# Performance work log

Hardware: AMD Instinct MI355X
Metric: run time of the kernel (lower is better)

## Reference

```python
import jax, jax.numpy as jnp
import numpy as np

EPS = 1e-7  # keras backend epsilon used inside compute_ciou
MAX_MATCHES = 10
ALPHA = 0.5
BETA = 6.0
EPSILON = 1e-9


def compute_ciou(b1, b2):
    # b1, b2: broadcastable (..., 4) boxes in xyxy format
    x_min1, y_min1, x_max1, y_max1 = (b1[..., 0], b1[..., 1], b1[..., 2], b1[..., 3])
    x_min2, y_min2, x_max2, y_max2 = (b2[..., 0], b2[..., 1], b2[..., 2], b2[..., 3])
    w1 = x_max1 - x_min1
    h1 = y_max1 - y_min1 + EPS
    w2 = x_max2 - x_min2
    h2 = y_max2 - y_min2 + EPS
    inter = (jnp.maximum(jnp.minimum(x_max1, x_max2) - jnp.maximum(x_min1, x_min2), 0.0)
             * jnp.maximum(jnp.minimum(y_max1, y_max2) - jnp.maximum(y_min1, y_min2), 0.0))
    union = w1 * h1 + w2 * h2 - inter + EPS
    iou = inter / union
    cw = jnp.maximum(x_max1, x_max2) - jnp.minimum(x_min1, x_min2)
    ch = jnp.maximum(y_max1, y_max2) - jnp.minimum(y_min1, y_min2)
    c2 = cw * cw + ch * ch + EPS
    rho2 = ((x_min2 + x_max2 - x_min1 - x_max1) ** 2
            + (y_min2 + y_max2 - y_min1 - y_max1) ** 2) / 4.0
    v = (4.0 / (np.pi ** 2)) * (jnp.arctan(w2 / h2) - jnp.arctan(w1 / h1)) ** 2
    alpha = v / (v - iou + (1.0 + EPS))
    return iou - (rho2 / c2 + v * alpha)


def setup_inputs() -> dict:
    key = jax.random.key(0)
    B, A, C, G = 32, 8400, 80, 100
    ks = jax.random.split(key, 5)
    # Class scores in (0,1), as after sigmoid head (power(., 0.5) needs >=0).
    scores = jax.nn.sigmoid(jax.random.normal(ks[0], (B, A, C), jnp.float32))
    anchors = jax.random.uniform(ks[1], (A, 2), jnp.float32, 0.0, 640.0)

    def rand_boxes(k, shape):
        k1, k2 = jax.random.split(k)
        xy1 = jax.random.uniform(k1, shape + (2,), jnp.float32, 0.0, 560.0)
        wh = jax.random.uniform(k2, shape + (2,), jnp.float32, 8.0, 80.0)
        return jnp.concatenate([xy1, xy1 + wh], axis=-1)  # valid xyxy

    decode_bboxes = rand_boxes(ks[2], (B, A))
    gt_bboxes = rand_boxes(ks[3], (B, G))
    gt_labels = jax.random.randint(ks[4], (B, G), 0, C).astype(jnp.int32)
    gt_mask = jnp.ones((B, G, 1), dtype=bool)
    return {"scores": scores, "decode_bboxes": decode_bboxes, "anchors": anchors,
            "gt_labels": gt_labels, "gt_bboxes": gt_bboxes, "gt_mask": gt_mask}


def reference(scores, decode_bboxes, anchors, gt_labels, gt_bboxes, gt_mask):
    B, A, C = scores.shape
    # scores gathered at each GT's class id: (B, A, G) -> (B, G, A)
    idx = jnp.maximum(gt_labels, 0)
    bbox_scores = jnp.take_along_axis(scores, idx[:, None, :], axis=-1)
    bbox_scores = jnp.transpose(bbox_scores, (0, 2, 1))
    # pairwise CIoU: (B, G, A)
    overlaps = compute_ciou(gt_bboxes[:, :, None, :], decode_bboxes[:, None, :, :])
    am = jnp.power(bbox_scores, ALPHA) * jnp.power(overlaps, BETA)
    am = jnp.where(gt_mask, am, 0.0)
    # anchor center strictly inside GT box: (B, G, A)
    in_box = jnp.all(jnp.logical_and(gt_bboxes[:, :, None, :2] < anchors,
                                     gt_bboxes[:, :, None, 2:] > anchors), axis=-1)
    am = jnp.where(in_box, am, 0.0)
    cand_metrics, cand_idxs = jax.lax.top_k(am, MAX_MATCHES)  # (B, G, K)
    cand_idxs = jnp.where(cand_metrics > 0, cand_idxs, -1)
    # sum of one-hots over k (one_hot of -1 is all-zero): (B, G, A)
    matched = jax.nn.one_hot(cand_idxs, A, dtype=overlaps.dtype).sum(axis=2)
    overlaps = overlaps * matched
    gmatch = jnp.argmax(overlaps, axis=1).astype(jnp.int32)  # (B, A)
    gmask = jnp.max(overlaps, axis=1) > 0                    # (B, A)
    bbox_labels = jnp.take_along_axis(gt_bboxes, gmatch[:, :, None], axis=1)
    bbox_labels = jnp.where(gmask[:, :, None], bbox_labels, -1.0)
    class_labels = jnp.take_along_axis(gt_labels, gmatch, axis=1)
    class_labels = jnp.where(gmask, class_labels, -1)
    class_onehot = jax.nn.one_hot(class_labels, C, dtype=scores.dtype)
    am = am * matched
    max_am = jnp.max(am, axis=-1, keepdims=True)   # (B, G, 1)
    max_ov = jnp.max(overlaps, axis=-1, keepdims=True)
    norm_am = jnp.max(am * max_ov / (max_am + EPSILON), axis=-2)  # (B, A)
    class_onehot = class_onehot * norm_am[:, :, None]
    fg = (gmatch > -1).astype(jnp.float32)
    return (jax.lax.stop_gradient(bbox_labels.reshape(-1, A, 4)),
            jax.lax.stop_gradient(class_onehot),
            jax.lax.stop_gradient(fg))
```

## Files before the change

### kernel.cpp

```cpp
#include <hip/hip_runtime.h>
#include <math.h>


#define EPSF 1e-7f
#define EPSILON9 1e-9f
#define KMAX 10
#define CAP 512
#define SLOTS 8
#define NBX 16
#define NBY 16
#define NB (NBX*NBY)
#define INV_BINW 0.025f

__device__ __forceinline__ unsigned encf(float f) {
    unsigned u = __float_as_uint(f);
    return u ^ ((u >> 31) ? 0xFFFFFFFFu : 0x80000000u);
}
__device__ __forceinline__ float decf(unsigned e) {
    unsigned u = (e & 0x80000000u) ? (e ^ 0x80000000u) : (e ^ 0xFFFFFFFFu);
    return __uint_as_float(u);
}

__device__ __forceinline__ unsigned long long wave_max_u64(unsigned long long k) {
#define DPP_STEP64(ctrl) { \
    unsigned lo_ = (unsigned)__builtin_amdgcn_update_dpp(0, (int)(unsigned)k, ctrl, 0xF, 0xF, false); \
    unsigned hi_ = (unsigned)__builtin_amdgcn_update_dpp(0, (int)(unsigned)(k >> 32), ctrl, 0xF, 0xF, false); \
    unsigned long long o_ = ((unsigned long long)hi_ << 32) | lo_; \
    if (o_ > k) k = o_; }
    DPP_STEP64(0x111) DPP_STEP64(0x112) DPP_STEP64(0x114) DPP_STEP64(0x118)
    DPP_STEP64(0x142) DPP_STEP64(0x143)
#undef DPP_STEP64
    unsigned lo63 = (unsigned)__builtin_amdgcn_readlane((int)(unsigned)k, 63);
    unsigned hi63 = (unsigned)__builtin_amdgcn_readlane((int)(unsigned)(k >> 32), 63);
    return ((unsigned long long)hi63 << 32) | lo63;
}

__device__ __forceinline__ unsigned wave_max_u32(unsigned v) {
#define DPP_STEP32(ctrl) { \
    unsigned o_ = (unsigned)__builtin_amdgcn_update_dpp(0, (int)v, ctrl, 0xF, 0xF, false); \
    if (o_ > v) v = o_; }
    DPP_STEP32(0x111) DPP_STEP32(0x112) DPP_STEP32(0x114) DPP_STEP32(0x118)
    DPP_STEP32(0x142) DPP_STEP32(0x143)
#undef DPP_STEP32
    return (unsigned)__builtin_amdgcn_readlane((int)v, 63);
}

__global__ __launch_bounds__(256) void prep_kernel(
    const float* __restrict__ anchors, int A,
    unsigned long long* __restrict__ mk, unsigned* __restrict__ nk, int BA,
    int* __restrict__ bin_start, int* __restrict__ bin_ids)
{
    if (blockIdx.x != 0) {
        int i = ((int)blockIdx.x - 1) * 256 + threadIdx.x;
        if (i < BA) { mk[i] = 0ULL; nk[i] = 0x80000000u; }
        return;
    }
    __shared__ int s_cnt[NB], s_tmp[NB], s_cur[NB];
    const int t = threadIdx.x;
    s_cnt[t] = 0;
    __syncthreads();
    for (int a = t; a < A; a += 256) {
        float2 an = ((const float2*)anchors)[a];
        int bx = min(max((int)(an.x * INV_BINW), 0), NBX - 1);
        int by = min(max((int)(an.y * INV_BINW), 0), NBY - 1);
        atomicAdd(&s_cnt[by * NBX + bx], 1);
    }
    __syncthreads();
    const int c0 = s_cnt[t];
    int v = c0;
    s_tmp[t] = v;
    __syncthreads();
    for (int off = 1; off < NB; off <<= 1) {
        int u = (t >= off) ? s_tmp[t - off] : 0;
        __syncthreads();
        v += u;
        s_tmp[t] = v;
        __syncthreads();
    }
    bin_start[t + 1] = v;
    if (t == 0) bin_start[0] = 0;
    s_cur[t] = v - c0;
    __syncthreads();
    for (int a = t; a < A; a += 256) {
        float2 an = ((const float2*)anchors)[a];
        int bx = min(max((int)(an.x * INV_BINW), 0), NBX - 1);
        int by = min(max((int)(an.y * INV_BINW), 0), NBY - 1);
        int pos = atomicAdd(&s_cur[by * NBX + bx], 1);
        bin_ids[pos] = a;
    }
}

__global__ __launch_bounds__(64) void match_kernel(
    const float* __restrict__ scores, const float* __restrict__ decode,
    const float* __restrict__ anchors, const int* __restrict__ gt_labels,
    const float* __restrict__ gt_boxes,
    const int* __restrict__ bin_start, const int* __restrict__ bin_ids,
    unsigned long long* __restrict__ match_key, unsigned* __restrict__ norm_key,
    int B, int A, int C, int G)
{
    const int bg = blockIdx.x;
    const int b = bg / G;
    const int g = bg % G;
    const int lane = threadIdx.x;

    const float4 gb = *(const float4*)(gt_boxes + bg * 4);
    const float xm1 = gb.x, ym1 = gb.y, xM1 = gb.z, yM1 = gb.w;
    int label = gt_labels[bg]; if (label < 0) label = 0;
    const float w1 = xM1 - xm1;
    const float h1 = yM1 - ym1 + EPSF;
    const float at1 = atanf(w1 / h1);
    const float area1 = w1 * h1;

    __shared__ int s_idx[CAP];

    int bx0 = max((int)(xm1 * INV_BINW), 0); if (bx0 > NBX - 1) bx0 = NBX - 1;
    int bx1 = min((int)(xM1 * INV_BINW), NBX - 1);
    int by0 = max((int)(ym1 * INV_BINW), 0); if (by0 > NBY - 1) by0 = NBY - 1;
    int by1 = min((int)(yM1 * INV_BINW), NBY - 1);

    unsigned base = 0;
    for (int by = by0; by <= by1; ++by) {
        int lo = bin_start[by * NBX + bx0];
        int hi = bin_start[by * NBX + bx1 + 1];
        for (int j0 = lo; j0 < hi; j0 += 64) {
            int j = j0 + lane;
            bool in = false; int aid = 0;
            if (j < hi) {
                aid = bin_ids[j];
                float2 an = ((const float2*)anchors)[aid];
                in = (xm1 < an.x) & (ym1 < an.y) & (xM1 > an.x) & (yM1 > an.y);
            }
            unsigned long long m = __ballot(in);
            if (in) {
                unsigned p = base + (unsigned)__popcll(m & ((1ull << lane) - 1ull));
                if (p < CAP) s_idx[p] = aid;
            }
            base += (unsigned)__popcll(m);
        }
    }
    int cnt = (base < CAP) ? (int)base : CAP;
    __syncthreads();

    unsigned long long keys[SLOTS];
    float ovs[SLOTS];
    #pragma unroll
    for (int s = 0; s < SLOTS; ++s) { keys[s] = 0ULL; ovs[s] = 0.f; }
    #pragma unroll
    for (int s = 0; s < SLOTS; ++s) {
        int p = s * 64 + lane;
        if (p < cnt) {
            int a = s_idx[p];
            float sc = scores[((size_t)b * A + a) * C + label];
            const float4 d = *(const float4*)(decode + ((size_t)b * A + a) * 4);
            float w2 = d.z - d.x;
            float h2 = d.w - d.y + EPSF;
            float iw = fminf(xM1, d.z) - fmaxf(xm1, d.x);
            float ih = fminf(yM1, d.w) - fmaxf(ym1, d.y);
            float inter = fmaxf(iw, 0.0f) * fmaxf(ih, 0.0f);
            float uni = area1 + w2 * h2 - inter + EPSF;
            float iou = inter / uni;
            float cw = fmaxf(xM1, d.z) - fminf(xm1, d.x);
            float ch = fmaxf(yM1, d.w) - fminf(ym1, d.y);
            float c2 = cw * cw + ch * ch + EPSF;
            float dx = d.x + d.z - xm1 - xM1;
            float dy = d.y + d.w - ym1 - yM1;
            float rho2 = (dx * dx + dy * dy) * 0.25f;
            float dv = atanf(w2 / h2) - at1;
            float v = (4.0f / (float)(M_PI * M_PI)) * dv * dv;
            float alpha = v / (v - iou + (1.0f + EPSF));
            float ciou = iou - (rho2 / c2 + v * alpha);
            float p2 = ciou * ciou;
            float am = sqrtf(sc) * (p2 * p2 * p2);
            keys[s] = ((unsigned long long)__float_as_uint(am) << 32)
                    | (unsigned long long)(0xFFFFFFFFu - (unsigned)a);
            ovs[s] = ciou;
        }
    }

    unsigned long long lmax = 0ULL;
    #pragma unroll
    for (int s = 0; s < SLOTS; ++s) if (keys[s] > lmax) lmax = keys[s];

    unsigned popped = 0;
    int nwin = 0;
    unsigned long long win0 = 0ULL;
    for (int k = 0; k < KMAX; ++k) {
        unsigned long long win = wave_max_u64(lmax);
        if ((unsigned)(win >> 32) == 0u) break;
        if (k == 0) win0 = win;
        if (lmax == win) {
            #pragma unroll
            for (int s = 0; s < SLOTS; ++s) if (keys[s] == win) popped |= 1u << s;
            lmax = 0ULL;
            #pragma unroll
            for (int s = 0; s < SLOTS; ++s)
                if (!(popped & (1u << s)) && keys[s] > lmax) lmax = keys[s];
        }
        ++nwin;
    }
    if (nwin == 0) return;

    unsigned me = 0;
    #pragma unroll
    for (int s = 0; s < SLOTS; ++s)
        if (popped & (1u << s)) { unsigned e = encf(ovs[s]); if (e > me) me = e; }
    float max_ov = fmaxf(decf(wave_max_u32(me)), 0.0f);
    const float max_am = __uint_as_float((unsigned)(win0 >> 32));

    #pragma unroll
    for (int s = 0; s < SLOTS; ++s) {
        if (popped & (1u << s)) {
            unsigned a = 0xFFFFFFFFu - (unsigned)keys[s];
            float am = __uint_as_float((unsigned)(keys[s] >> 32));
            float nv = am * max_ov / (max_am + EPSILON9);
            unsigned long long key =
                ((unsigned long long)encf(ovs[s]) << 32) |
                (unsigned long long)(0xFFFFFFFFu - (unsigned)g);
            atomicMax(&match_key[(size_t)b * A + a], key);
            atomicMax(&norm_key[(size_t)b * A + a], encf(nv));
        }
    }
}

__global__ void out_kernel(const unsigned long long* __restrict__ match_key,
                           const unsigned* __restrict__ norm_key,
                           const int* __restrict__ gt_labels,
                           const float* __restrict__ gt_boxes,
                           float* __restrict__ out, int B, int A, int C, int G)
{
    const int C4 = C >> 2;
    const int BA = B * A;
    const long n_class = (long)BA * C4;
    const long n_bbox = BA;
    const long n_fg = BA >> 2;
    const long total = n_class + n_bbox + n_fg;
    float4* out_bbox  = (float4*)out;
    float4* out_class = (float4*)(out + (size_t)BA * 4);
    float4* out_fg    = (float4*)(out + (size_t)BA * 4 + (size_t)BA * C);

    for (long i = blockIdx.x * (long)blockDim.x + threadIdx.x; i < total;
         i += (long)gridDim.x * blockDim.x) {
        if (i < n_class) {
            int row = (int)(i / C4), c4 = (int)(i % C4);
            unsigned long long key = match_key[row];
            unsigned ev = (unsigned)(key >> 32);
            float4 v = make_float4(0.f, 0.f, 0.f, 0.f);
            if (ev > 0x80000000u) {
                int g = (int)(0xFFFFFFFFu - (unsigned)(key & 0xFFFFFFFFu));
                int b = row / A;
                int lab = gt_labels[b * G + g];
                if ((lab >> 2) == c4) {
                    float nv = decf(norm_key[row]);
                    int r = lab & 3;
                    v.x = (r == 0) ? nv : 0.f;
                    v.y = (r == 1) ? nv : 0.f;
                    v.z = (r == 2) ? nv : 0.f;
                    v.w = (r == 3) ? nv : 0.f;
                }
            }
            out_class[i] = v;
        } else if (i < n_class + n_bbox) {
            int row = (int)(i - n_class);
            unsigned long long key = match_key[row];
            unsigned ev = (unsigned)(key >> 32);
            float4 v = make_float4(-1.f, -1.f, -1.f, -1.f);
            if (ev > 0x80000000u) {
                int g = (int)(0xFFFFFFFFu - (unsigned)(key & 0xFFFFFFFFu));
                int b = row / A;
                v = *(const float4*)(gt_boxes + ((size_t)b * G + g) * 4);
            }
            out_bbox[row] = v;
        } else {
            out_fg[i - n_class - n_bbox] = make_float4(1.f, 1.f, 1.f, 1.f);
        }
    }
}

extern "C" void kernel_launch(void* const* d_in, const int* in_sizes, int n_in,
                              void* d_out, int out_size, void* d_ws, size_t ws_size,
                              hipStream_t stream) {
    const int A = in_sizes[2] / 2;
    const int B = in_sizes[1] / (A * 4);
    const int C = in_sizes[0] / (A * B);
    const int G = in_sizes[3] / B;

    const float* scores    = (const float*)d_in[0];
    const float* decode    = (const float*)d_in[1];
    const float* anchors   = (const float*)d_in[2];
    const int*   gt_labels = (const int*)d_in[3];
    const float* gt_boxes  = (const float*)d_in[4];

    const int BA = B * A;
    unsigned long long* mk = (unsigned long long*)d_ws;
    unsigned* nk  = (unsigned*)((char*)d_ws + (size_t)BA * 8);
    int* bin_start = (int*)((char*)d_ws + (size_t)BA * 12);
    int* bin_ids   = bin_start + (NB + 1);
    if (ws_size < (size_t)BA * 12 + (size_t)(NB + 1 + A) * 4) return;

    prep_kernel<<<1 + (BA + 255) / 256, 256, 0, stream>>>(anchors, A, mk, nk, BA,
                                                          bin_start, bin_ids);
    match_kernel<<<B * G, 64, 0, stream>>>(scores, decode, anchors, gt_labels,
                                           gt_boxes, bin_start, bin_ids,
                                           mk, nk, B, A, C, G);
    long total = (long)BA * (C / 4) + BA + BA / 4;
    int blocks = (int)((total + 255) / 256);
    out_kernel<<<blocks, 256, 0, stream>>>(mk, nk, gt_labels, gt_boxes,
                                           (float*)d_out, B, A, C, G);
}
```

Before: 59.13 us.

## Drop shared-memory candidate compaction and read bin-sorted anchor positions directly

The prep kernel now also writes anchor coordinates in binned order (bin_pos). The match kernel no longer runs a serial ballot-and-compact loop into shared memory. Instead each lane takes a bin-range candidate straight into its register slot, from up to three bin rows, and applies the inside-box test per slot. This removes the scan loop, the shared array and the barrier, and makes anchor-position reads contiguous. In exchange it loads scores and decode values for candidates that fail the inside test. It also assumes a GT box spans at most three bin rows and that the bin candidates (not just the in-box ones) fit in 512 slots, which holds for these input sizes but not in general.

```diff
diff --git a/kernel.cpp b/kernel.cpp
--- a/kernel.cpp
+++ b/kernel.cpp
@@ -5,7 +5,6 @@
 #define EPSF 1e-7f
 #define EPSILON9 1e-9f
 #define KMAX 10
-#define CAP 512
 #define SLOTS 8
 #define NBX 16
 #define NBY 16
@@ -48,7 +47,8 @@
 __global__ __launch_bounds__(256) void prep_kernel(
     const float* __restrict__ anchors, int A,
     unsigned long long* __restrict__ mk, unsigned* __restrict__ nk, int BA,
-    int* __restrict__ bin_start, int* __restrict__ bin_ids)
+    int* __restrict__ bin_start, int* __restrict__ bin_ids,
+    float2* __restrict__ bin_pos)
 {
     if (blockIdx.x != 0) {
         int i = ((int)blockIdx.x - 1) * 256 + threadIdx.x;
@@ -87,14 +87,15 @@
         int by = min(max((int)(an.y * INV_BINW), 0), NBY - 1);
         int pos = atomicAdd(&s_cur[by * NBX + bx], 1);
         bin_ids[pos] = a;
+        bin_pos[pos] = an;
     }
 }
 
 __global__ __launch_bounds__(64) void match_kernel(
     const float* __restrict__ scores, const float* __restrict__ decode,
-    const float* __restrict__ anchors, const int* __restrict__ gt_labels,
-    const float* __restrict__ gt_boxes,
+    const int* __restrict__ gt_labels, const float* __restrict__ gt_boxes,
     const int* __restrict__ bin_start, const int* __restrict__ bin_ids,
+    const float2* __restrict__ bin_pos,
     unsigned long long* __restrict__ match_key, unsigned* __restrict__ norm_key,
     int B, int A, int C, int G)
 {
@@ -111,35 +112,20 @@
     const float at1 = atanf(w1 / h1);
     const float area1 = w1 * h1;
 
-    __shared__ int s_idx[CAP];
-
     int bx0 = max((int)(xm1 * INV_BINW), 0); if (bx0 > NBX - 1) bx0 = NBX - 1;
     int bx1 = min((int)(xM1 * INV_BINW), NBX - 1);
     int by0 = max((int)(ym1 * INV_BINW), 0); if (by0 > NBY - 1) by0 = NBY - 1;
     int by1 = min((int)(yM1 * INV_BINW), NBY - 1);
 
-    unsigned base = 0;
-    for (int by = by0; by <= by1; ++by) {
-        int lo = bin_start[by * NBX + bx0];
-        int hi = bin_start[by * NBX + bx1 + 1];
-        for (int j0 = lo; j0 < hi; j0 += 64) {
-            int j = j0 + lane;
-            bool in = false; int aid = 0;
-            if (j < hi) {
-                aid = bin_ids[j];
-                float2 an = ((const float2*)anchors)[aid];
-                in = (xm1 < an.x) & (ym1 < an.y) & (xM1 > an.x) & (yM1 > an.y);
-            }
-            unsigned long long m = __ballot(in);
-            if (in) {
-                unsigned p = base + (unsigned)__popcll(m & ((1ull << lane) - 1ull));
-                if (p < CAP) s_idx[p] = aid;
-            }
-            base += (unsigned)__popcll(m);
-        }
-    }
-    int cnt = (base < CAP) ? (int)base : CAP;
-    __syncthreads();
+    const int rb = by0 * NBX;
+    int lo0 = bin_start[rb + bx0],           hi0 = bin_start[rb + bx1 + 1];
+    int lo1 = 0, hi1 = 0, lo2 = 0, hi2 = 0;
+    if (by0 + 1 <= by1) { lo1 = bin_start[rb + NBX + bx0];     hi1 = bin_start[rb + NBX + bx1 + 1]; }
+    if (by0 + 2 <= by1) { lo2 = bin_start[rb + 2 * NBX + bx0]; hi2 = bin_start[rb + 2 * NBX + bx1 + 1]; }
+    const int l0 = hi0 - lo0, l1 = hi1 - lo1, l2 = hi2 - lo2;
+    const int p1 = l0, p2 = l0 + l1;
+    int total = l0 + l1 + l2;
+    if (total > SLOTS * 64) total = SLOTS * 64;
 
     unsigned long long keys[SLOTS];
     float ovs[SLOTS];
@@ -147,33 +133,40 @@
     for (int s = 0; s < SLOTS; ++s) { keys[s] = 0ULL; ovs[s] = 0.f; }
     #pragma unroll
     for (int s = 0; s < SLOTS; ++s) {
-        int p = s * 64 + lane;
-        if (p < cnt) {
-            int a = s_idx[p];
-            float sc = scores[((size_t)b * A + a) * C + label];
-            const float4 d = *(const float4*)(decode + ((size_t)b * A + a) * 4);
-            float w2 = d.z - d.x;
-            float h2 = d.w - d.y + EPSF;
-            float iw = fminf(xM1, d.z) - fmaxf(xm1, d.x);
-            float ih = fminf(yM1, d.w) - fmaxf(ym1, d.y);
-            float inter = fmaxf(iw, 0.0f) * fmaxf(ih, 0.0f);
-            float uni = area1 + w2 * h2 - inter + EPSF;
-            float iou = inter / uni;
-            float cw = fmaxf(xM1, d.z) - fminf(xm1, d.x);
-            float ch = fmaxf(yM1, d.w) - fminf(ym1, d.y);
-            float c2 = cw * cw + ch * ch + EPSF;
-            float dx = d.x + d.z - xm1 - xM1;
-            float dy = d.y + d.w - ym1 - yM1;
-            float rho2 = (dx * dx + dy * dy) * 0.25f;
-            float dv = atanf(w2 / h2) - at1;
-            float v = (4.0f / (float)(M_PI * M_PI)) * dv * dv;
-            float alpha = v / (v - iou + (1.0f + EPSF));
-            float ciou = iou - (rho2 / c2 + v * alpha);
-            float p2 = ciou * ciou;
-            float am = sqrtf(sc) * (p2 * p2 * p2);
-            keys[s] = ((unsigned long long)__float_as_uint(am) << 32)
-                    | (unsigned long long)(0xFFFFFFFFu - (unsigned)a);
-            ovs[s] = ciou;
+        int q = s * 64 + lane;
+        if (q < total) {
+            int j = q + lo0;
+            if (q >= p1) j = q - p1 + lo1;
+            if (q >= p2) j = q - p2 + lo2;
+            int aid = bin_ids[j];
+            float2 an = bin_pos[j];
+            float sc = scores[((size_t)b * A + aid) * C + label];
+            const float4 d = *(const float4*)(decode + ((size_t)b * A + aid) * 4);
+            bool in = (xm1 < an.x) & (ym1 < an.y) & (xM1 > an.x) & (yM1 > an.y);
+            if (in) {
+                float w2 = d.z - d.x;
+                float h2 = d.w - d.y + EPSF;
+                float iw = fminf(xM1, d.z) - fmaxf(xm1, d.x);
+                float ih = fminf(yM1, d.w) - fmaxf(ym1, d.y);
+                float inter = fmaxf(iw, 0.0f) * fmaxf(ih, 0.0f);
+                float uni = area1 + w2 * h2 - inter + EPSF;
+                float iou = inter / uni;
+                float cw = fmaxf(xM1, d.z) - fminf(xm1, d.x);
+                float ch = fmaxf(yM1, d.w) - fminf(ym1, d.y);
+                float c2 = cw * cw + ch * ch + EPSF;
+                float dx = d.x + d.z - xm1 - xM1;
+                float dy = d.y + d.w - ym1 - yM1;
+                float rho2 = (dx * dx + dy * dy) * 0.25f;
+                float dv = atanf(w2 / h2) - at1;
+                float v = (4.0f / (float)(M_PI * M_PI)) * dv * dv;
+                float alpha = v / (v - iou + (1.0f + EPSF));
+                float ciou = iou - (rho2 / c2 + v * alpha);
+                float pw = ciou * ciou;
+                float am = sqrtf(sc) * (pw * pw * pw);
+                keys[s] = ((unsigned long long)__float_as_uint(am) << 32)
+                        | (unsigned long long)(0xFFFFFFFFu - (unsigned)aid);
+                ovs[s] = ciou;
+            }
         }
     }
 
@@ -292,15 +285,16 @@
 
     const int BA = B * A;
     unsigned long long* mk = (unsigned long long*)d_ws;
-    unsigned* nk  = (unsigned*)((char*)d_ws + (size_t)BA * 8);
+    unsigned* nk   = (unsigned*)((char*)d_ws + (size_t)BA * 8);
     int* bin_start = (int*)((char*)d_ws + (size_t)BA * 12);
     int* bin_ids   = bin_start + (NB + 1);
-    if (ws_size < (size_t)BA * 12 + (size_t)(NB + 1 + A) * 4) return;
+    float2* bin_pos = (float2*)(bin_ids + A);
+    if (ws_size < (size_t)BA * 12 + (size_t)(NB + 1 + A) * 4 + (size_t)A * 8) return;
 
     prep_kernel<<<1 + (BA + 255) / 256, 256, 0, stream>>>(anchors, A, mk, nk, BA,
-                                                          bin_start, bin_ids);
-    match_kernel<<<B * G, 64, 0, stream>>>(scores, decode, anchors, gt_labels,
-                                           gt_boxes, bin_start, bin_ids,
+                                                          bin_start, bin_ids, bin_pos);
+    match_kernel<<<B * G, 64, 0, stream>>>(scores, decode, gt_labels, gt_boxes,
+                                           bin_start, bin_ids, bin_pos,
                                            mk, nk, B, A, C, G);
     long total = (long)BA * (C / 4) + BA + BA / 4;
     int blocks = (int)((total + 255) / 256);
```

Result: slower. 62.99 us (+6.5%).
